# Kernel tuning notes

Hardware: AMD Instinct MI355X
Metric: run time of the kernel (lower is better)

Reference implementation:

```python
import jax, jax.numpy as jnp
import numpy as np
from jax import lax

B, C, P, H = 4, 3, 160, 32          # batch of box patches, channels, patch size, score-net hidden
TEMB = 64                            # time-embedding dim
BETA0, BETA1 = 0.1, 20.0             # subVP SDE beta_min / beta_max
T_EPS = 1e-5                         # integration start time (timesteps=(1e-5, 1))
N_STEPS = 10                         # (1 - eps) / ode_step_size with step_size=0.1


def _conv(x, w, b):
    y = lax.conv_general_dilated(x, w, (1, 1), 'SAME',
                                 dimension_numbers=('NCHW', 'OIHW', 'NCHW'))
    return y + b[None, :, None, None]


def _time_emb(t):
    half = TEMB // 2
    freqs = jnp.exp(-np.log(10000.0) / (half - 1) * jnp.arange(half, dtype=jnp.float32))
    a = t[:, None] * 999.0 * freqs[None, :]   # continuous t scaled as in score_sde
    return jnp.concatenate([jnp.sin(a), jnp.cos(a)], axis=-1)


def _score_net(x, t, params):
    w1, b1, wt, bt, w2, b2, w3, b3 = params
    emb = _time_emb(t) @ wt + bt                       # [B, H]
    h = jax.nn.relu(_conv(x, w1, b1) + emb[:, :, None, None])
    h = jax.nn.relu(_conv(h, w2, b2))
    return _conv(h, w3, b3)


def _drift(x, tvec, params):
    # subVP probability-flow ODE drift: f(x,t) - 0.5 * g(t)^2 * score(x,t)
    bd = BETA1 - BETA0
    beta_t = BETA0 + tvec * bd
    lmc = -0.25 * tvec ** 2 * bd - 0.5 * tvec * BETA0   # log mean coeff
    std = 1.0 - jnp.exp(2.0 * lmc)                      # marginal std
    g2 = beta_t * (1.0 - jnp.exp(4.0 * lmc))            # diffusion^2
    score = _score_net(x, tvec, params) / std[:, None, None, None]
    return -0.5 * beta_t[:, None, None, None] * x - 0.5 * g2[:, None, None, None] * score


def _forward(patches, hs_epsilon, params):
    eps = jnp.broadcast_to(hs_epsilon, patches.shape)   # fixed Rademacher probe
    dt = (1.0 - T_EPS) / N_STEPS

    def rhs(x, t):
        tvec = jnp.ones((x.shape[0],), x.dtype) * t
        # Skilling-Hutchinson divergence: eps^T J eps via one jvp
        drift, jv = jax.jvp(lambda xx: _drift(xx, tvec, params), (x,), (eps,))
        return drift, jnp.sum(jv * eps, axis=(1, 2, 3))

    def step(carry, t0):
        x, lp = carry
        k1x, k1l = rhs(x, t0)
        k2x, k2l = rhs(x + 0.5 * dt * k1x, t0 + 0.5 * dt)
        k3x, k3l = rhs(x + 0.5 * dt * k2x, t0 + 0.5 * dt)
        k4x, k4l = rhs(x + dt * k3x, t0 + dt)
        x = x + (dt / 6.0) * (k1x + 2.0 * k2x + 2.0 * k3x + k4x)
        lp = lp + (dt / 6.0) * (k1l + 2.0 * k2l + 2.0 * k3l + k4l)
        return (x, lp), None

    ts = T_EPS + dt * jnp.arange(N_STEPS, dtype=patches.dtype)
    init = (patches, jnp.zeros((patches.shape[0],), patches.dtype))
    (z, delta_logp), _ = lax.scan(jax.checkpoint(step), init, ts)

    Ndim = float(np.prod(patches.shape[1:]))
    prior_logp = -0.5 * Ndim * np.log(2.0 * np.pi) - 0.5 * jnp.sum(z ** 2, axis=(1, 2, 3))
    bpd = -(prior_logp + delta_logp) / np.log(2.0)
    return bpd / Ndim                                   # per-patch NLL (bits/dim)


def setup_inputs() -> dict:
    key = jax.random.key(0)
    ks = jax.random.split(key, 6)
    s = 0.05
    return {
        'patches': jax.random.normal(ks[0], (B, C, P, P), jnp.float32),
        'hs_epsilon': jnp.sign(jax.random.normal(ks[1], (1, C, P, P), jnp.float32)),
        'w1': jax.random.normal(ks[2], (H, C, 3, 3), jnp.float32) * s,
        'b1': jnp.zeros((H,), jnp.float32),
        'wt': jax.random.normal(ks[3], (TEMB, H), jnp.float32) * s,
        'bt': jnp.zeros((H,), jnp.float32),
        'w2': jax.random.normal(ks[4], (H, H, 3, 3), jnp.float32) * s,
        'b2': jnp.zeros((H,), jnp.float32),
        'w3': jax.random.normal(ks[5], (C, H, 3, 3), jnp.float32) * s,
        'b3': jnp.zeros((C,), jnp.float32),
    }


def reference(patches, hs_epsilon, w1, b1, wt, bt, w2, b2, w3, b3):
    params = (w1, b1, wt, bt, w2, b2, w3, b3)
    return _forward(patches, hs_epsilon, params)
```

## Files before the change

kernel.cpp:

```cpp
#include <hip/hip_runtime.h>
#include <hip/hip_bf16.h>
#include <math.h>

#define PW 160
#define PSQ 25600
#define NB 4
#define NX 307200
#define NDIM 76800

#define TY 10
#define TX 20
#define XH 16
#define XW 26
#define XSZ 416
#define H1H 14
#define H1W 24
#define H1N 336
#define H2H 12
#define H2W 22
#define H2N 264
#define OUTN 200

typedef __attribute__((ext_vector_type(8))) short short8;
typedef __attribute__((ext_vector_type(4))) float float4v;

struct TS40 { float t[40]; };
struct MC40 { float m[40]; float A; };

__device__ __forceinline__ short bf16s(float f) {
    return __builtin_bit_cast(short, __float2bfloat16(f));
}
__device__ __forceinline__ unsigned packbf(float a, float b) {
    return (unsigned)(unsigned short)bf16s(a) | ((unsigned)(unsigned short)bf16s(b) << 16);
}

__global__ void emb_kernel(const float* __restrict__ wt, const float* __restrict__ bt,
                           float* __restrict__ emb, TS40 ts) {
    int r = blockIdx.x, k = threadIdx.x;
    __shared__ float e64[64];
    float t = ts.t[r];
    int j = k & 31;
    float freq = expf(-0.29710775393471556f * (float)j);
    float a = t * 999.0f * freq;
    e64[k] = (k < 32) ? sinf(a) : cosf(a);
    __syncthreads();
    if (k < 32) {
        float acc = bt[k];
        #pragma unroll 8
        for (int q = 0; q < 64; q++) acc += e64[q] * wt[q * 32 + k];
        emb[r * 32 + k] = acc;
    }
}

__global__ void repack_kernel(const float* __restrict__ w1, const float* __restrict__ w2,
                              const float* __restrict__ w3, short* __restrict__ w1p,
                              short* __restrict__ w2p, short* __restrict__ w3p) {
    int tid = blockIdx.x * 256 + threadIdx.x;
    if (tid < 9216) {
        int j = tid & 7, co = (tid >> 3) & 31, q4 = tid >> 8;
        int tap = q4 >> 2, quad = q4 & 3, ci = quad * 8 + j;
        w2p[tid] = bf16s(w2[(co * 32 + ci) * 9 + tap]);
    }
    if (tid < 4608) {
        int j = tid & 7, co = (tid >> 3) & 15, q4 = tid >> 7;
        int tap = q4 >> 2, quad = q4 & 3, ci = quad * 8 + j;
        float v = (co < 3) ? w3[(co * 32 + ci) * 9 + tap] : 0.0f;
        w3p[tid] = bf16s(v);
    }
    if (tid < 1024) {
        int j = tid & 7, co = (tid >> 3) & 31, quad = tid >> 8;
        int k = quad * 8 + j;
        float v = 0.0f;
        if (k < 27) { int tap = (k * 11) >> 5; int ci = k - tap * 3; v = w1[(co * 3 + ci) * 9 + tap]; }
        w1p[tid] = bf16s(v);
    }
}

__global__ __launch_bounds__(256) void teps_conv1(
    const float* __restrict__ xin, const short* __restrict__ w1p,
    short* __restrict__ outH) {
    const int tile = blockIdx.x;
    const int ty0 = (tile / 10) * 16, tx0 = (tile % 10) * 16;
    const int tid = threadIdx.x;
    const int lane = tid & 63, wv = tid >> 6;
    const int n = lane & 15, quad = lane >> 4;
    __shared__ float sX[3 * 324];
    for (int idx = tid; idx < 3 * 324; idx += 256) {
        int ci = idx / 324, p = idx - ci * 324;
        int ly = p / 18, lx = p - ly * 18;
        int gy = ty0 + ly - 1, gx = tx0 + lx - 1;
        float v = 0.0f;
        if (gy >= 0 && gy < PW && gx >= 0 && gx < PW)
            v = xin[(size_t)ci * PSQ + gy * PW + gx];
        sX[idx] = v;
    }
    __syncthreads();
    int offj[8], valj[8];
    #pragma unroll
    for (int j = 0; j < 8; ++j) {
        int k = quad * 8 + j;
        valj[j] = (k < 27);
        int tap = (k * 11) >> 5; if (k >= 27) tap = 0;
        int ci = k - tap * 3;
        int dy = (tap * 11) >> 5, dx = tap - dy * 3;
        offj[j] = valj[j] ? (ci * 324 + dy * 18 + dx + n) : 0;
    }
    short8 a0 = *(const short8*)&w1p[(quad * 32 + n) * 8];
    short8 a1 = *(const short8*)&w1p[(quad * 32 + 16 + n) * 8];
    #pragma unroll
    for (int r = 0; r < 4; ++r) {
        int row = wv * 4 + r;
        short8 bb;
        #pragma unroll
        for (int j = 0; j < 8; ++j) {
            float v = valj[j] ? sX[offj[j] + row * 18] : 0.0f;
            bb[j] = bf16s(v);
        }
        float4v acc0 = {0.f, 0.f, 0.f, 0.f}, acc1 = {0.f, 0.f, 0.f, 0.f};
        acc0 = __builtin_amdgcn_mfma_f32_16x16x32_bf16(a0, bb, acc0, 0, 0, 0);
        acc1 = __builtin_amdgcn_mfma_f32_16x16x32_bf16(a1, bb, acc1, 0, 0, 0);
        int pix = (ty0 + row) * PW + tx0 + n;
        uint2 h0, h1v;
        h0.x = packbf(acc0[0], acc0[1]); h0.y = packbf(acc0[2], acc0[3]);
        h1v.x = packbf(acc1[0], acc1[1]); h1v.y = packbf(acc1[2], acc1[3]);
        *(uint2*)&outH[(size_t)pix * 32 + quad * 4] = h0;
        *(uint2*)&outH[(size_t)pix * 32 + 16 + quad * 4] = h1v;
    }
}

__global__ __launch_bounds__(256, 2) void fused_stage(
    const float* __restrict__ xin, float* __restrict__ x0,
    float* __restrict__ xacc, float* __restrict__ xst,
    const short* __restrict__ w1p, const short* __restrict__ w2p,
    const short* __restrict__ w3p, const float* __restrict__ b1,
    const float* __restrict__ b2, const float* __restrict__ b3,
    const float* __restrict__ embr, const short* __restrict__ tepsb,
    const float* __restrict__ epsin, float* __restrict__ Sacc,
    float c1, float c2, float dt, int mode) {
    const int bid = blockIdx.x;
    const int tile = ((bid & 7) << 4) | (bid >> 3);
    const int b = blockIdx.y;
    const int oy = (tile >> 3) * TY, ox = (tile & 7) * TX;
    const int tid = threadIdx.x;
    const int lane = tid & 63, wv = tid >> 6;
    const int n = lane & 15, quad = lane >> 4;

    __shared__ __align__(16) char smem[77088];
    short* sH1 = (short*)smem;
    short* sD1 = (short*)(smem + 21504);
    short* sH2 = (short*)(smem + 43008);
    short* sD2 = (short*)(smem + 59904);
    short* sX  = (short*)(smem + 43008);
    float* sOut = (float*)smem;
    float* sBE = (float*)(smem + 76800);
    float* sB2 = (float*)(smem + 76928);
    float* sB3 = (float*)(smem + 77056);
    float* wsum = (float*)(smem + 77068);

    if (tid < 32) { sBE[tid] = b1[tid] + embr[tid]; sB2[tid] = b2[tid]; }
    if (tid < 3) sB3[tid] = b3[tid];

    for (int idx = tid; idx < 3 * XSZ; idx += 256) {
        int ci = idx / XSZ, p = idx - ci * XSZ;
        int ly = p / XW, lx = p - ly * XW;
        int gy = oy - 3 + ly, gx = ox - 3 + lx;
        float v = 0.0f;
        if (gy >= 0 && gy < PW && gx >= 0 && gx < PW)
            v = xin[(size_t)(b * 3 + ci) * PSQ + gy * PW + gx];
        sX[idx] = bf16s(v);
    }
    __syncthreads();

    {
        int koff[8], kval[8];
        #pragma unroll
        for (int j = 0; j < 8; ++j) {
            int k = quad * 8 + j;
            kval[j] = (k < 27);
            int tap = (k * 11) >> 5; if (k >= 27) tap = 0;
            int ci = k - tap * 3;
            int dy = (tap * 11) >> 5, dx = tap - dy * 3;
            koff[j] = kval[j] ? (ci * XSZ + dy * XW + dx) : 0;
        }
        short8 a0 = *(const short8*)&w1p[(quad * 32 + n) * 8];
        short8 a1 = *(const short8*)&w1p[(quad * 32 + 16 + n) * 8];
        for (int t = wv; t < 21; t += 4) {
            int p = t * 16 + n;
            int ry = p / H1W, rx = p - ry * H1W;
            int gy = oy - 2 + ry, gx = ox - 2 + rx;
            int inimg = (gy >= 0 && gy < PW && gx >= 0 && gx < PW);
            size_t tbase = inimg ? ((size_t)(gy * PW + gx) * 32) : 0;
            uint2 t20 = *(const uint2*)&tepsb[tbase + quad * 4];
            uint2 t21 = *(const uint2*)&tepsb[tbase + 16 + quad * 4];
            int base = ry * XW + rx;
            short8 bb;
            #pragma unroll
            for (int j = 0; j < 8; ++j)
                bb[j] = kval[j] ? sX[koff[j] + base] : (short)0;
            float4v acc0 = {0.f, 0.f, 0.f, 0.f}, acc1 = {0.f, 0.f, 0.f, 0.f};
            acc0 = __builtin_amdgcn_mfma_f32_16x16x32_bf16(a0, bb, acc0, 0, 0, 0);
            acc1 = __builtin_amdgcn_mfma_f32_16x16x32_bf16(a1, bb, acc1, 0, 0, 0);
            int swz = (p & 7) << 4;
            #pragma unroll
            for (int mt = 0; mt < 2; ++mt) {
                float4v* ac = mt ? &acc1 : &acc0;
                uint2 t2 = mt ? t21 : t20;
                int co0 = mt * 16 + quad * 4;
                unsigned ts4[4] = {t2.x & 0xFFFFu, t2.x >> 16, t2.y & 0xFFFFu, t2.y >> 16};
                unsigned hv[4], dv[4];
                #pragma unroll
                for (int g = 0; g < 4; ++g) {
                    float pre = (*ac)[g] + sBE[co0 + g];
                    hv[g] = inimg ? (unsigned)(unsigned short)bf16s(fmaxf(pre, 0.0f)) : 0u;
                    dv[g] = (inimg && pre > 0.0f) ? ts4[g] : 0u;
                }
                uint2 hw, dw;
                hw.x = hv[0] | (hv[1] << 16); hw.y = hv[2] | (hv[3] << 16);
                dw.x = dv[0] | (dv[1] << 16); dw.y = dv[2] | (dv[3] << 16);
                int byw = ((p << 6) | (co0 << 1)) ^ swz;
                *(uint2*)((char*)sH1 + byw) = hw;
                *(uint2*)((char*)sD1 + byw) = dw;
            }
        }
    }
    __syncthreads();

    {
        short8 a2[9][2];
        #pragma unroll
        for (int tap = 0; tap < 9; ++tap) {
            a2[tap][0] = *(const short8*)&w2p[((tap * 4 + quad) * 32 + n) * 8];
            a2[tap][1] = *(const short8*)&w2p[((tap * 4 + quad) * 32 + 16 + n) * 8];
        }
        for (int t = wv; t < 17; t += 4) {
            int p = t * 16 + n;
            int pc = p < H2N ? p : (H2N - 1);
            int ry = pc / H2W, rx = pc - ry * H2W;
            float4v aP0 = {0.f,0.f,0.f,0.f}, aP1 = {0.f,0.f,0.f,0.f};
            float4v aD0 = {0.f,0.f,0.f,0.f}, aD1 = {0.f,0.f,0.f,0.f};
            #pragma unroll
            for (int tap = 0; tap < 9; ++tap) {
                int dy = (tap * 11) >> 5, dx = tap - dy * 3;
                int q = (ry + dy) * H1W + rx + dx;
                int byr = ((q << 6) | (quad << 4)) ^ ((q & 7) << 4);
                short8 bp = *(const short8*)((const char*)sH1 + byr);
                short8 bd = *(const short8*)((const char*)sD1 + byr);
                aP0 = __builtin_amdgcn_mfma_f32_16x16x32_bf16(a2[tap][0], bp, aP0, 0, 0, 0);
                aP1 = __builtin_amdgcn_mfma_f32_16x16x32_bf16(a2[tap][1], bp, aP1, 0, 0, 0);
                aD0 = __builtin_amdgcn_mfma_f32_16x16x32_bf16(a2[tap][0], bd, aD0, 0, 0, 0);
                aD1 = __builtin_amdgcn_mfma_f32_16x16x32_bf16(a2[tap][1], bd, aD1, 0, 0, 0);
            }
            int gy = oy - 1 + ry, gx = ox - 1 + rx;
            int inimg = (gy >= 0 && gy < PW && gx >= 0 && gx < PW);
            if (p < H2N) {
                int swz = (p & 7) << 4;
                #pragma unroll
                for (int mt = 0; mt < 2; ++mt) {
                    float4v* acP = mt ? &aP1 : &aP0;
                    float4v* acD = mt ? &aD1 : &aD0;
                    int co0 = mt * 16 + quad * 4;
                    unsigned hv[4], dv[4];
                    #pragma unroll
                    for (int g = 0; g < 4; ++g) {
                        float pre = (*acP)[g] + sB2[co0 + g];
                        hv[g] = inimg ? (unsigned)(unsigned short)bf16s(fmaxf(pre, 0.0f)) : 0u;
                        dv[g] = (inimg && pre > 0.0f) ? (unsigned)(unsigned short)bf16s((*acD)[g]) : 0u;
                    }
                    uint2 hw, dw;
                    hw.x = hv[0] | (hv[1] << 16); hw.y = hv[2] | (hv[3] << 16);
                    dw.x = dv[0] | (dv[1] << 16); dw.y = dv[2] | (dv[3] << 16);
                    int byw = ((p << 6) | (co0 << 1)) ^ swz;
                    *(uint2*)((char*)sH2 + byw) = hw;
                    *(uint2*)((char*)sD2 + byw) = dw;
                }
            }
        }
    }
    __syncthreads();

    float pf_x[3], pf_e[3], pf_a[3], pf_x0[3];
    #pragma unroll
    for (int rep = 0; rep < 3; ++rep) {
        int idx = tid + rep * 256;
        int v = (idx < 3 * OUTN);
        int idc = v ? idx : 0;
        int c = idc / OUTN, pp = idc - c * OUTN;
        int ry = pp / TX, rx = pp - ry * TX;
        int pix = (oy + ry) * PW + ox + rx;
        size_t gi = (size_t)(b * 3 + c) * PSQ + pix;
        pf_x[rep] = v ? xin[gi] : 0.0f;
        pf_e[rep] = v ? epsin[c * PSQ + pix] : 0.0f;
        pf_a[rep] = 0.0f; pf_x0[rep] = 0.0f;
        if (mode >= 1) {
            pf_a[rep] = v ? xacc[gi] : 0.0f;
            pf_x0[rep] = v ? x0[gi] : 0.0f;
        }
    }

    {
        short8 a3[9];
        #pragma unroll
        for (int tap = 0; tap < 9; ++tap)
            a3[tap] = *(const short8*)&w3p[((tap * 4 + quad) * 16 + n) * 8];
        for (int t = wv; t < 13; t += 4) {
            int p = t * 16 + n;
            int pc = p < OUTN ? p : (OUTN - 1);
            int ry = pc / TX, rx = pc - ry * TX;
            float4v aP = {0.f,0.f,0.f,0.f}, aD = {0.f,0.f,0.f,0.f};
            #pragma unroll
            for (int tap = 0; tap < 9; ++tap) {
                int dy = (tap * 11) >> 5, dx = tap - dy * 3;
                int q = (ry + dy) * H2W + rx + dx;
                int byr = ((q << 6) | (quad << 4)) ^ ((q & 7) << 4);
                short8 bp = *(const short8*)((const char*)sH2 + byr);
                short8 bd = *(const short8*)((const char*)sD2 + byr);
                aP = __builtin_amdgcn_mfma_f32_16x16x32_bf16(a3[tap], bp, aP, 0, 0, 0);
                aD = __builtin_amdgcn_mfma_f32_16x16x32_bf16(a3[tap], bd, aD, 0, 0, 0);
            }
            if (quad == 0 && p < OUTN) {
                #pragma unroll
                for (int c = 0; c < 3; ++c) {
                    sOut[c * OUTN + p] = aP[c] + sB3[c];
                    sOut[3 * OUTN + c * OUTN + p] = aD[c];
                }
            }
        }
    }
    __syncthreads();

    float s = 0.0f;
    #pragma unroll
    for (int rep = 0; rep < 3; ++rep) {
        int idx = tid + rep * 256;
        if (idx < 3 * OUTN) {
            int c = idx / OUTN, pp = idx - c * OUTN;
            int ry = pp / TX, rx = pp - ry * TX;
            int pix = (oy + ry) * PW + ox + rx;
            size_t gi = (size_t)(b * 3 + c) * PSQ + pix;
            float y = sOut[c * OUTN + pp];
            float d = sOut[3 * OUTN + c * OUTN + pp];
            float xv = pf_x[rep];
            float k = -c1 * xv - c2 * y;
            if (mode == 0) {
                xacc[gi] = k;
                xst[gi] = xv + 0.5f * dt * k;
            } else if (mode == 1) {
                xacc[gi] = pf_a[rep] + 2.0f * k;
                xst[gi] = pf_x0[rep] + 0.5f * dt * k;
            } else if (mode == 2) {
                xacc[gi] = pf_a[rep] + 2.0f * k;
                xst[gi] = pf_x0[rep] + dt * k;
            } else {
                x0[gi] = pf_x0[rep] + (dt / 6.0f) * (pf_a[rep] + k);
            }
            s += d * pf_e[rep];
        }
    }
    #pragma unroll
    for (int off = 32; off > 0; off >>= 1) s += __shfl_down(s, off);
    if (lane == 0) wsum[wv] = s;
    __syncthreads();
    if (tid == 0) atomicAdd(&Sacc[b], wsum[0] + wsum[1] + wsum[2] + wsum[3]);
}

__global__ void sumz2_kernel(const float* __restrict__ x0, float* __restrict__ sumz2) {
    int b = blockIdx.x, seg = blockIdx.y, tid = threadIdx.x;
    const float* p = x0 + (size_t)b * NDIM + seg * 3072;
    float s = 0.0f;
    for (int i = tid; i < 3072; i += 256) { float v = p[i]; s += v * v; }
    #pragma unroll
    for (int off = 32; off > 0; off >>= 1) s += __shfl_down(s, off);
    __shared__ float wsum[4];
    if ((tid & 63) == 0) wsum[tid >> 6] = s;
    __syncthreads();
    if (tid == 0) atomicAdd(&sumz2[b], wsum[0] + wsum[1] + wsum[2] + wsum[3]);
}

__global__ void bpd_kernel(const float* __restrict__ S, const float* __restrict__ sumz2,
                           float* __restrict__ out, MC40 mc) {
    int b = threadIdx.x;
    if (b >= NB) return;
    float lp = mc.A;
    for (int r = 0; r < 40; r++) lp -= mc.m[r] * S[r * 4 + b];
    float prior = -70574.479354f - 0.5f * sumz2[b];
    out[b] = -(prior + lp) * 1.8785164100960743e-5f;
}

extern "C" void kernel_launch(void* const* d_in, const int* in_sizes, int n_in,
                              void* d_out, int out_size, void* d_ws, size_t ws_size,
                              hipStream_t stream) {
    const float* patches = (const float*)d_in[0];
    const float* epsin = (const float*)d_in[1];
    const float* w1 = (const float*)d_in[2];
    const float* b1 = (const float*)d_in[3];
    const float* wt = (const float*)d_in[4];
    const float* bt = (const float*)d_in[5];
    const float* w2 = (const float*)d_in[6];
    const float* b2 = (const float*)d_in[7];
    const float* w3 = (const float*)d_in[8];
    const float* b3 = (const float*)d_in[9];
    float* outp = (float*)d_out;
    char* wsb = (char*)d_ws;

    float* Sbuf  = (float*)(wsb + 0);
    float* sumz2 = (float*)(wsb + 640);
    float* emb   = (float*)(wsb + 1024);
    short* w1p   = (short*)(wsb + 6144);
    short* w2p   = (short*)(wsb + 8192);
    short* w3p   = (short*)(wsb + 26624);
    short* tepsb = (short*)(wsb + 36864);
    float* x0    = (float*)(wsb + 1675264);
    float* xacc  = (float*)(wsb + 2904064);
    float* xst   = (float*)(wsb + 4132864);

    const double dt = (1.0 - 1e-5) / 10.0;
    TS40 ts; MC40 mc;
    float c1a[40], c2a[40];
    double A = 0.0;
    const double wgt[4] = {1.0, 2.0, 2.0, 1.0};
    for (int i = 0; i < 10; i++) {
        double t0 = 1e-5 + dt * i;
        double tr[4] = {t0, t0 + 0.5 * dt, t0 + 0.5 * dt, t0 + dt};
        for (int s = 0; s < 4; s++) {
            int r = i * 4 + s;
            double t = tr[s];
            double beta = 0.1 + 19.9 * t;
            double lmc = -0.25 * t * t * 19.9 - 0.05 * t;
            double stdv = 1.0 - exp(2.0 * lmc);
            double g2 = beta * (1.0 - exp(4.0 * lmc));
            double c2 = 0.5 * g2 / stdv;
            ts.t[r] = (float)t;
            c1a[r] = (float)(0.5 * beta);
            c2a[r] = (float)c2;
            double coef = dt / 6.0 * wgt[s];
            mc.m[r] = (float)(coef * c2);
            A += coef * (-0.5 * beta * (double)NDIM);
        }
    }
    mc.A = (float)A;

    hipMemsetAsync(wsb, 0, 656, stream);
    hipMemcpyAsync(x0, patches, NX * sizeof(float), hipMemcpyDeviceToDevice, stream);

    emb_kernel<<<40, 64, 0, stream>>>(wt, bt, emb, ts);
    repack_kernel<<<36, 256, 0, stream>>>(w1, w2, w3, w1p, w2p, w3p);
    teps_conv1<<<100, 256, 0, stream>>>(epsin, w1p, tepsb);

    for (int i = 0; i < 10; i++) {
        for (int s = 0; s < 4; s++) {
            int r = i * 4 + s;
            const float* xin = (s == 0) ? x0 : xst;
            fused_stage<<<dim3(128, NB), 256, 0, stream>>>(
                xin, x0, xacc, xst, w1p, w2p, w3p, b1, b2, b3,
                emb + r * 32, tepsb, epsin, Sbuf + r * 4,
                c1a[r], c2a[r], (float)dt, s);
        }
    }
    sumz2_kernel<<<dim3(NB, 25), 256, 0, stream>>>(x0, sumz2);
    bpd_kernel<<<1, 64, 0, stream>>>(Sbuf, sumz2, outp, mc);
}
```

Before: 948.3 us.

## Fuse all RK4 stages into one persistent kernel with grid barriers

Replaces the 40 per-stage launches with a single persistent kernel of 512 blocks. Blocks synchronise between stages through an atomic counter barrier in global memory. Weights, the conv1 tangent (eps) result and the eps values are loaded once into registers and reused across all stages, and the separate teps_conv1 kernel is removed. This cuts launch overhead and repeated weight loads, but it relies on all 512 blocks being co-resident and adds spin-wait barrier cost plus register pressure.

Measured after the change: 3.790 ms. 300% more time.

```diff
diff --git a/kernel.cpp b/kernel.cpp
--- a/kernel.cpp
+++ b/kernel.cpp
@@ -7,16 +7,13 @@
 #define NB 4
 #define NX 307200
 #define NDIM 76800
+#define NBLK 512
 
 #define TY 10
 #define TX 20
-#define XH 16
 #define XW 26
 #define XSZ 416
-#define H1H 14
 #define H1W 24
-#define H1N 336
-#define H2H 12
 #define H2W 22
 #define H2N 264
 #define OUTN 200
@@ -26,6 +23,7 @@
 
 struct TS40 { float t[40]; };
 struct MC40 { float m[40]; float A; };
+struct PK { float c1[40]; float c2[40]; };
 
 __device__ __forceinline__ short bf16s(float f) {
     return __builtin_bit_cast(short, __float2bfloat16(f));
@@ -76,67 +74,14 @@
     }
 }
 
-__global__ __launch_bounds__(256) void teps_conv1(
-    const float* __restrict__ xin, const short* __restrict__ w1p,
-    short* __restrict__ outH) {
-    const int tile = blockIdx.x;
-    const int ty0 = (tile / 10) * 16, tx0 = (tile % 10) * 16;
-    const int tid = threadIdx.x;
-    const int lane = tid & 63, wv = tid >> 6;
-    const int n = lane & 15, quad = lane >> 4;
-    __shared__ float sX[3 * 324];
-    for (int idx = tid; idx < 3 * 324; idx += 256) {
-        int ci = idx / 324, p = idx - ci * 324;
-        int ly = p / 18, lx = p - ly * 18;
-        int gy = ty0 + ly - 1, gx = tx0 + lx - 1;
-        float v = 0.0f;
-        if (gy >= 0 && gy < PW && gx >= 0 && gx < PW)
-            v = xin[(size_t)ci * PSQ + gy * PW + gx];
-        sX[idx] = v;
-    }
-    __syncthreads();
-    int offj[8], valj[8];
-    #pragma unroll
-    for (int j = 0; j < 8; ++j) {
-        int k = quad * 8 + j;
-        valj[j] = (k < 27);
-        int tap = (k * 11) >> 5; if (k >= 27) tap = 0;
-        int ci = k - tap * 3;
-        int dy = (tap * 11) >> 5, dx = tap - dy * 3;
-        offj[j] = valj[j] ? (ci * 324 + dy * 18 + dx + n) : 0;
-    }
-    short8 a0 = *(const short8*)&w1p[(quad * 32 + n) * 8];
-    short8 a1 = *(const short8*)&w1p[(quad * 32 + 16 + n) * 8];
-    #pragma unroll
-    for (int r = 0; r < 4; ++r) {
-        int row = wv * 4 + r;
-        short8 bb;
-        #pragma unroll
-        for (int j = 0; j < 8; ++j) {
-            float v = valj[j] ? sX[offj[j] + row * 18] : 0.0f;
-            bb[j] = bf16s(v);
-        }
-        float4v acc0 = {0.f, 0.f, 0.f, 0.f}, acc1 = {0.f, 0.f, 0.f, 0.f};
-        acc0 = __builtin_amdgcn_mfma_f32_16x16x32_bf16(a0, bb, acc0, 0, 0, 0);
-        acc1 = __builtin_amdgcn_mfma_f32_16x16x32_bf16(a1, bb, acc1, 0, 0, 0);
-        int pix = (ty0 + row) * PW + tx0 + n;
-        uint2 h0, h1v;
-        h0.x = packbf(acc0[0], acc0[1]); h0.y = packbf(acc0[2], acc0[3]);
-        h1v.x = packbf(acc1[0], acc1[1]); h1v.y = packbf(acc1[2], acc1[3]);
-        *(uint2*)&outH[(size_t)pix * 32 + quad * 4] = h0;
-        *(uint2*)&outH[(size_t)pix * 32 + 16 + quad * 4] = h1v;
-    }
-}
-
-__global__ __launch_bounds__(256, 2) void fused_stage(
-    const float* __restrict__ xin, float* __restrict__ x0,
-    float* __restrict__ xacc, float* __restrict__ xst,
+__global__ __launch_bounds__(256, 2) void persist_kernel(
+    float* __restrict__ x0, float* __restrict__ xacc, float* __restrict__ xst,
     const short* __restrict__ w1p, const short* __restrict__ w2p,
     const short* __restrict__ w3p, const float* __restrict__ b1,
     const float* __restrict__ b2, const float* __restrict__ b3,
-    const float* __restrict__ embr, const short* __restrict__ tepsb,
-    const float* __restrict__ epsin, float* __restrict__ Sacc,
-    float c1, float c2, float dt, int mode) {
+    const float* __restrict__ emb, const float* __restrict__ epsin,
+    float* __restrict__ Sacc, unsigned* __restrict__ bars,
+    PK pk, float dt) {
     const int bid = blockIdx.x;
     const int tile = ((bid & 7) << 4) | (bid >> 3);
     const int b = blockIdx.y;
@@ -157,8 +102,22 @@
     float* sB3 = (float*)(smem + 77056);
     float* wsum = (float*)(smem + 77068);
 
-    if (tid < 32) { sBE[tid] = b1[tid] + embr[tid]; sB2[tid] = b2[tid]; }
+    float myb1 = (tid < 32) ? b1[tid] : 0.0f;
+    if (tid < 32) sB2[tid] = b2[tid];
     if (tid < 3) sB3[tid] = b3[tid];
+
+    int koff[8], kval[8];
+    #pragma unroll
+    for (int j = 0; j < 8; ++j) {
+        int k = quad * 8 + j;
+        kval[j] = (k < 27);
+        int tap = (k * 11) >> 5; if (k >= 27) tap = 0;
+        int ci = k - tap * 3;
+        int dy = (tap * 11) >> 5, dx = tap - dy * 3;
+        koff[j] = kval[j] ? (ci * XSZ + dy * XW + dx) : 0;
+    }
+    short8 a0 = *(const short8*)&w1p[(quad * 32 + n) * 8];
+    short8 a1w = *(const short8*)&w1p[(quad * 32 + 16 + n) * 8];
 
     for (int idx = tid; idx < 3 * XSZ; idx += 256) {
         int ci = idx / XSZ, p = idx - ci * XSZ;
@@ -166,32 +125,19 @@
         int gy = oy - 3 + ly, gx = ox - 3 + lx;
         float v = 0.0f;
         if (gy >= 0 && gy < PW && gx >= 0 && gx < PW)
-            v = xin[(size_t)(b * 3 + ci) * PSQ + gy * PW + gx];
+            v = epsin[(size_t)ci * PSQ + gy * PW + gx];
         sX[idx] = bf16s(v);
     }
     __syncthreads();
-
-    {
-        int koff[8], kval[8];
-        #pragma unroll
-        for (int j = 0; j < 8; ++j) {
-            int k = quad * 8 + j;
-            kval[j] = (k < 27);
-            int tap = (k * 11) >> 5; if (k >= 27) tap = 0;
-            int ci = k - tap * 3;
-            int dy = (tap * 11) >> 5, dx = tap - dy * 3;
-            koff[j] = kval[j] ? (ci * XSZ + dy * XW + dx) : 0;
-        }
-        short8 a0 = *(const short8*)&w1p[(quad * 32 + n) * 8];
-        short8 a1 = *(const short8*)&w1p[(quad * 32 + 16 + n) * 8];
-        for (int t = wv; t < 21; t += 4) {
+    uint2 pt0[6], pt1[6];
+    #pragma unroll
+    for (int it = 0; it < 6; ++it) { pt0[it].x = pt0[it].y = 0u; pt1[it].x = pt1[it].y = 0u; }
+    #pragma unroll
+    for (int it = 0; it < 6; ++it) {
+        int t = wv + it * 4;
+        if (t < 21) {
             int p = t * 16 + n;
             int ry = p / H1W, rx = p - ry * H1W;
-            int gy = oy - 2 + ry, gx = ox - 2 + rx;
-            int inimg = (gy >= 0 && gy < PW && gx >= 0 && gx < PW);
-            size_t tbase = inimg ? ((size_t)(gy * PW + gx) * 32) : 0;
-            uint2 t20 = *(const uint2*)&tepsb[tbase + quad * 4];
-            uint2 t21 = *(const uint2*)&tepsb[tbase + 16 + quad * 4];
             int base = ry * XW + rx;
             short8 bb;
             #pragma unroll
@@ -199,39 +145,94 @@
                 bb[j] = kval[j] ? sX[koff[j] + base] : (short)0;
             float4v acc0 = {0.f, 0.f, 0.f, 0.f}, acc1 = {0.f, 0.f, 0.f, 0.f};
             acc0 = __builtin_amdgcn_mfma_f32_16x16x32_bf16(a0, bb, acc0, 0, 0, 0);
-            acc1 = __builtin_amdgcn_mfma_f32_16x16x32_bf16(a1, bb, acc1, 0, 0, 0);
-            int swz = (p & 7) << 4;
-            #pragma unroll
-            for (int mt = 0; mt < 2; ++mt) {
-                float4v* ac = mt ? &acc1 : &acc0;
-                uint2 t2 = mt ? t21 : t20;
-                int co0 = mt * 16 + quad * 4;
-                unsigned ts4[4] = {t2.x & 0xFFFFu, t2.x >> 16, t2.y & 0xFFFFu, t2.y >> 16};
-                unsigned hv[4], dv[4];
+            acc1 = __builtin_amdgcn_mfma_f32_16x16x32_bf16(a1w, bb, acc1, 0, 0, 0);
+            pt0[it].x = packbf(acc0[0], acc0[1]); pt0[it].y = packbf(acc0[2], acc0[3]);
+            pt1[it].x = packbf(acc1[0], acc1[1]); pt1[it].y = packbf(acc1[2], acc1[3]);
+        }
+    }
+    __syncthreads();
+
+    float pf_e[3];
+    #pragma unroll
+    for (int rep = 0; rep < 3; ++rep) {
+        int idx = tid + rep * 256;
+        int v = (idx < 3 * OUTN);
+        int idc = v ? idx : 0;
+        int c = idc / OUTN, pp = idc - c * OUTN;
+        int ry = pp / TX, rx = pp - ry * TX;
+        pf_e[rep] = v ? epsin[(size_t)c * PSQ + (oy + ry) * PW + ox + rx] : 0.0f;
+    }
+
+    short8 a2[9][2];
+    #pragma unroll
+    for (int tap = 0; tap < 9; ++tap) {
+        a2[tap][0] = *(const short8*)&w2p[((tap * 4 + quad) * 32 + n) * 8];
+        a2[tap][1] = *(const short8*)&w2p[((tap * 4 + quad) * 32 + 16 + n) * 8];
+    }
+    short8 a3[9];
+    #pragma unroll
+    for (int tap = 0; tap < 9; ++tap)
+        a3[tap] = *(const short8*)&w3p[((tap * 4 + quad) * 16 + n) * 8];
+
+    #pragma unroll 1
+    for (int r = 0; r < 40; ++r) {
+        const int mode = r & 3;
+        const float c1 = pk.c1[r], c2 = pk.c2[r];
+        const float* xin = (mode == 0) ? x0 : xst;
+        if (tid < 32) sBE[tid] = myb1 + emb[r * 32 + tid];
+
+        for (int idx = tid; idx < 3 * XSZ; idx += 256) {
+            int ci = idx / XSZ, p = idx - ci * XSZ;
+            int ly = p / XW, lx = p - ly * XW;
+            int gy = oy - 3 + ly, gx = ox - 3 + lx;
+            float v = 0.0f;
+            if (gy >= 0 && gy < PW && gx >= 0 && gx < PW)
+                v = xin[(size_t)(b * 3 + ci) * PSQ + gy * PW + gx];
+            sX[idx] = bf16s(v);
+        }
+        __syncthreads();
+
+        #pragma unroll
+        for (int it = 0; it < 6; ++it) {
+            int t = wv + it * 4;
+            if (t < 21) {
+                int p = t * 16 + n;
+                int ry = p / H1W, rx = p - ry * H1W;
+                int gy = oy - 2 + ry, gx = ox - 2 + rx;
+                int inimg = (gy >= 0 && gy < PW && gx >= 0 && gx < PW);
+                int base = ry * XW + rx;
+                short8 bb;
                 #pragma unroll
-                for (int g = 0; g < 4; ++g) {
-                    float pre = (*ac)[g] + sBE[co0 + g];
-                    hv[g] = inimg ? (unsigned)(unsigned short)bf16s(fmaxf(pre, 0.0f)) : 0u;
-                    dv[g] = (inimg && pre > 0.0f) ? ts4[g] : 0u;
+                for (int j = 0; j < 8; ++j)
+                    bb[j] = kval[j] ? sX[koff[j] + base] : (short)0;
+                float4v acc0 = {0.f, 0.f, 0.f, 0.f}, acc1 = {0.f, 0.f, 0.f, 0.f};
+                acc0 = __builtin_amdgcn_mfma_f32_16x16x32_bf16(a0, bb, acc0, 0, 0, 0);
+                acc1 = __builtin_amdgcn_mfma_f32_16x16x32_bf16(a1w, bb, acc1, 0, 0, 0);
+                int swz = (p & 7) << 4;
+                #pragma unroll
+                for (int mt = 0; mt < 2; ++mt) {
+                    float4v* ac = mt ? &acc1 : &acc0;
+                    uint2 t2 = mt ? pt1[it] : pt0[it];
+                    int co0 = mt * 16 + quad * 4;
+                    unsigned ts4[4] = {t2.x & 0xFFFFu, t2.x >> 16, t2.y & 0xFFFFu, t2.y >> 16};
+                    unsigned hv[4], dv[4];
+                    #pragma unroll
+                    for (int g = 0; g < 4; ++g) {
+                        float pre = (*ac)[g] + sBE[co0 + g];
+                        hv[g] = inimg ? (unsigned)(unsigned short)bf16s(fmaxf(pre, 0.0f)) : 0u;
+                        dv[g] = (inimg && pre > 0.0f) ? ts4[g] : 0u;
+                    }
+                    uint2 hw, dw;
+                    hw.x = hv[0] | (hv[1] << 16); hw.y = hv[2] | (hv[3] << 16);
+                    dw.x = dv[0] | (dv[1] << 16); dw.y = dv[2] | (dv[3] << 16);
+                    int byw = ((p << 6) | (co0 << 1)) ^ swz;
+                    *(uint2*)((char*)sH1 + byw) = hw;
+                    *(uint2*)((char*)sD1 + byw) = dw;
                 }
-                uint2 hw, dw;
-                hw.x = hv[0] | (hv[1] << 16); hw.y = hv[2] | (hv[3] << 16);
-                dw.x = dv[0] | (dv[1] << 16); dw.y = dv[2] | (dv[3] << 16);
-                int byw = ((p << 6) | (co0 << 1)) ^ swz;
-                *(uint2*)((char*)sH1 + byw) = hw;
-                *(uint2*)((char*)sD1 + byw) = dw;
-            }
-        }
-    }
-    __syncthreads();
-
-    {
-        short8 a2[9][2];
-        #pragma unroll
-        for (int tap = 0; tap < 9; ++tap) {
-            a2[tap][0] = *(const short8*)&w2p[((tap * 4 + quad) * 32 + n) * 8];
-            a2[tap][1] = *(const short8*)&w2p[((tap * 4 + quad) * 32 + 16 + n) * 8];
-        }
+            }
+        }
+        __syncthreads();
+
         for (int t = wv; t < 17; t += 4) {
             int p = t * 16 + n;
             int pc = p < H2N ? p : (H2N - 1);
@@ -275,33 +276,25 @@
                 }
             }
         }
-    }
-    __syncthreads();
-
-    float pf_x[3], pf_e[3], pf_a[3], pf_x0[3];
-    #pragma unroll
-    for (int rep = 0; rep < 3; ++rep) {
-        int idx = tid + rep * 256;
-        int v = (idx < 3 * OUTN);
-        int idc = v ? idx : 0;
-        int c = idc / OUTN, pp = idc - c * OUTN;
-        int ry = pp / TX, rx = pp - ry * TX;
-        int pix = (oy + ry) * PW + ox + rx;
-        size_t gi = (size_t)(b * 3 + c) * PSQ + pix;
-        pf_x[rep] = v ? xin[gi] : 0.0f;
-        pf_e[rep] = v ? epsin[c * PSQ + pix] : 0.0f;
-        pf_a[rep] = 0.0f; pf_x0[rep] = 0.0f;
-        if (mode >= 1) {
-            pf_a[rep] = v ? xacc[gi] : 0.0f;
-            pf_x0[rep] = v ? x0[gi] : 0.0f;
-        }
-    }
-
-    {
-        short8 a3[9];
+        __syncthreads();
+
+        float pf_x[3], pf_a[3], pf_x0[3];
         #pragma unroll
-        for (int tap = 0; tap < 9; ++tap)
-            a3[tap] = *(const short8*)&w3p[((tap * 4 + quad) * 16 + n) * 8];
+        for (int rep = 0; rep < 3; ++rep) {
+            int idx = tid + rep * 256;
+            int v = (idx < 3 * OUTN);
+            int idc = v ? idx : 0;
+            int c = idc / OUTN, pp = idc - c * OUTN;
+            int ry = pp / TX, rx = pp - ry * TX;
+            size_t gi = (size_t)(b * 3 + c) * PSQ + (oy + ry) * PW + ox + rx;
+            pf_x[rep] = v ? xin[gi] : 0.0f;
+            pf_a[rep] = 0.0f; pf_x0[rep] = 0.0f;
+            if (mode >= 1) {
+                pf_a[rep] = v ? xacc[gi] : 0.0f;
+                pf_x0[rep] = v ? x0[gi] : 0.0f;
+            }
+        }
+
         for (int t = wv; t < 13; t += 4) {
             int p = t * 16 + n;
             int pc = p < OUTN ? p : (OUTN - 1);
@@ -325,42 +318,53 @@
                 }
             }
         }
-    }
-    __syncthreads();
-
-    float s = 0.0f;
-    #pragma unroll
-    for (int rep = 0; rep < 3; ++rep) {
-        int idx = tid + rep * 256;
-        if (idx < 3 * OUTN) {
-            int c = idx / OUTN, pp = idx - c * OUTN;
-            int ry = pp / TX, rx = pp - ry * TX;
-            int pix = (oy + ry) * PW + ox + rx;
-            size_t gi = (size_t)(b * 3 + c) * PSQ + pix;
-            float y = sOut[c * OUTN + pp];
-            float d = sOut[3 * OUTN + c * OUTN + pp];
-            float xv = pf_x[rep];
-            float k = -c1 * xv - c2 * y;
-            if (mode == 0) {
-                xacc[gi] = k;
-                xst[gi] = xv + 0.5f * dt * k;
-            } else if (mode == 1) {
-                xacc[gi] = pf_a[rep] + 2.0f * k;
-                xst[gi] = pf_x0[rep] + 0.5f * dt * k;
-            } else if (mode == 2) {
-                xacc[gi] = pf_a[rep] + 2.0f * k;
-                xst[gi] = pf_x0[rep] + dt * k;
-            } else {
-                x0[gi] = pf_x0[rep] + (dt / 6.0f) * (pf_a[rep] + k);
-            }
-            s += d * pf_e[rep];
-        }
-    }
-    #pragma unroll
-    for (int off = 32; off > 0; off >>= 1) s += __shfl_down(s, off);
-    if (lane == 0) wsum[wv] = s;
-    __syncthreads();
-    if (tid == 0) atomicAdd(&Sacc[b], wsum[0] + wsum[1] + wsum[2] + wsum[3]);
+        __syncthreads();
+
+        float s = 0.0f;
+        #pragma unroll
+        for (int rep = 0; rep < 3; ++rep) {
+            int idx = tid + rep * 256;
+            if (idx < 3 * OUTN) {
+                int c = idx / OUTN, pp = idx - c * OUTN;
+                int ry = pp / TX, rx = pp - ry * TX;
+                size_t gi = (size_t)(b * 3 + c) * PSQ + (oy + ry) * PW + ox + rx;
+                float y = sOut[c * OUTN + pp];
+                float d = sOut[3 * OUTN + c * OUTN + pp];
+                float xv = pf_x[rep];
+                float k = -c1 * xv - c2 * y;
+                if (mode == 0) {
+                    xacc[gi] = k;
+                    xst[gi] = xv + 0.5f * dt * k;
+                } else if (mode == 1) {
+                    xacc[gi] = pf_a[rep] + 2.0f * k;
+                    xst[gi] = pf_x0[rep] + 0.5f * dt * k;
+                } else if (mode == 2) {
+                    xacc[gi] = pf_a[rep] + 2.0f * k;
+                    xst[gi] = pf_x0[rep] + dt * k;
+                } else {
+                    x0[gi] = pf_x0[rep] + (dt / 6.0f) * (pf_a[rep] + k);
+                }
+                s += d * pf_e[rep];
+            }
+        }
+        #pragma unroll
+        for (int off = 32; off > 0; off >>= 1) s += __shfl_down(s, off);
+        if (lane == 0) wsum[wv] = s;
+        __syncthreads();
+        if (tid == 0) atomicAdd(&Sacc[r * 4 + b], wsum[0] + wsum[1] + wsum[2] + wsum[3]);
+
+        if (r < 39) {
+            __syncthreads();
+            if (tid == 0) {
+                __threadfence();
+                __hip_atomic_fetch_add(&bars[r], 1u, __ATOMIC_ACQ_REL, __HIP_MEMORY_SCOPE_AGENT);
+                while (__hip_atomic_load(&bars[r], __ATOMIC_ACQUIRE, __HIP_MEMORY_SCOPE_AGENT) < NBLK)
+                    __builtin_amdgcn_s_sleep(8);
+                __threadfence();
+            }
+            __syncthreads();
+        }
+    }
 }
 
 __global__ void sumz2_kernel(const float* __restrict__ x0, float* __restrict__ sumz2) {
@@ -404,18 +408,17 @@
 
     float* Sbuf  = (float*)(wsb + 0);
     float* sumz2 = (float*)(wsb + 640);
+    unsigned* bars = (unsigned*)(wsb + 768);
     float* emb   = (float*)(wsb + 1024);
     short* w1p   = (short*)(wsb + 6144);
     short* w2p   = (short*)(wsb + 8192);
     short* w3p   = (short*)(wsb + 26624);
-    short* tepsb = (short*)(wsb + 36864);
     float* x0    = (float*)(wsb + 1675264);
     float* xacc  = (float*)(wsb + 2904064);
     float* xst   = (float*)(wsb + 4132864);
 
     const double dt = (1.0 - 1e-5) / 10.0;
-    TS40 ts; MC40 mc;
-    float c1a[40], c2a[40];
+    TS40 ts; MC40 mc; PK pk;
     double A = 0.0;
     const double wgt[4] = {1.0, 2.0, 2.0, 1.0};
     for (int i = 0; i < 10; i++) {
@@ -430,8 +433,8 @@
             double g2 = beta * (1.0 - exp(4.0 * lmc));
             double c2 = 0.5 * g2 / stdv;
             ts.t[r] = (float)t;
-            c1a[r] = (float)(0.5 * beta);
-            c2a[r] = (float)c2;
+            pk.c1[r] = (float)(0.5 * beta);
+            pk.c2[r] = (float)c2;
             double coef = dt / 6.0 * wgt[s];
             mc.m[r] = (float)(coef * c2);
             A += coef * (-0.5 * beta * (double)NDIM);
@@ -439,23 +442,16 @@
     }
     mc.A = (float)A;
 
-    hipMemsetAsync(wsb, 0, 656, stream);
+    hipMemsetAsync(wsb, 0, 928, stream);
     hipMemcpyAsync(x0, patches, NX * sizeof(float), hipMemcpyDeviceToDevice, stream);
 
     emb_kernel<<<40, 64, 0, stream>>>(wt, bt, emb, ts);
     repack_kernel<<<36, 256, 0, stream>>>(w1, w2, w3, w1p, w2p, w3p);
-    teps_conv1<<<100, 256, 0, stream>>>(epsin, w1p, tepsb);
-
-    for (int i = 0; i < 10; i++) {
-        for (int s = 0; s < 4; s++) {
-            int r = i * 4 + s;
-            const float* xin = (s == 0) ? x0 : xst;
-            fused_stage<<<dim3(128, NB), 256, 0, stream>>>(
-                xin, x0, xacc, xst, w1p, w2p, w3p, b1, b2, b3,
-                emb + r * 32, tepsb, epsin, Sbuf + r * 4,
-                c1a[r], c2a[r], (float)dt, s);
-        }
-    }
+
+    persist_kernel<<<dim3(128, NB), 256, 0, stream>>>(
+        x0, xacc, xst, w1p, w2p, w3p, b1, b2, b3,
+        emb, epsin, Sbuf, bars, pk, (float)dt);
+
     sumz2_kernel<<<dim3(NB, 25), 256, 0, stream>>>(x0, sumz2);
     bpd_kernel<<<1, 64, 0, stream>>>(Sbuf, sumz2, outp, mc);
 }
```

## Double fused stage block to 512 threads and prefetch conv1 tangent loads

Applied to the files above, without the earlier changes.

Raises the fused RK stage kernel from 4 to 8 waves per block and redistributes the conv1/conv2/conv3 tile loops and epilogue across them. The tangent-conv1 global loads are hoisted to the kernel start so they overlap the input staging into shared memory. The aim is more latency hiding inside each block. The launch bound now asks for 4 blocks of 512 threads, which tightens register budgets and may force spills, and the ~77KB of shared memory per block still limits how many blocks fit per CU.

Result: faster. 858.9 us (-9.4%).

```diff
diff --git a/kernel.cpp b/kernel.cpp
--- a/kernel.cpp
+++ b/kernel.cpp
@@ -10,13 +10,9 @@
 
 #define TY 10
 #define TX 20
-#define XH 16
 #define XW 26
 #define XSZ 416
-#define H1H 14
 #define H1W 24
-#define H1N 336
-#define H2H 12
 #define H2W 22
 #define H2N 264
 #define OUTN 200
@@ -128,7 +124,7 @@
     }
 }
 
-__global__ __launch_bounds__(256, 2) void fused_stage(
+__global__ __launch_bounds__(512, 4) void fused_stage(
     const float* __restrict__ xin, float* __restrict__ x0,
     float* __restrict__ xacc, float* __restrict__ xst,
     const short* __restrict__ w1p, const short* __restrict__ w2p,
@@ -145,7 +141,7 @@
     const int lane = tid & 63, wv = tid >> 6;
     const int n = lane & 15, quad = lane >> 4;
 
-    __shared__ __align__(16) char smem[77088];
+    __shared__ __align__(16) char smem[77104];
     short* sH1 = (short*)smem;
     short* sD1 = (short*)(smem + 21504);
     short* sH2 = (short*)(smem + 43008);
@@ -155,12 +151,26 @@
     float* sBE = (float*)(smem + 76800);
     float* sB2 = (float*)(smem + 76928);
     float* sB3 = (float*)(smem + 77056);
-    float* wsum = (float*)(smem + 77068);
+    float* wsum = (float*)(smem + 77072);
+
+    uint2 pt0[3], pt1[3];
+    #pragma unroll
+    for (int it = 0; it < 3; ++it) {
+        int t = wv + it * 8;
+        int tt = (t < 21) ? t : 0;
+        int p = tt * 16 + n;
+        int ry = p / H1W, rx = p - ry * H1W;
+        int gy = oy - 2 + ry, gx = ox - 2 + rx;
+        int ok = (t < 21) && gy >= 0 && gy < PW && gx >= 0 && gx < PW;
+        size_t tbase = ok ? ((size_t)(gy * PW + gx) * 32) : 0;
+        pt0[it] = *(const uint2*)&tepsb[tbase + quad * 4];
+        pt1[it] = *(const uint2*)&tepsb[tbase + 16 + quad * 4];
+    }
 
     if (tid < 32) { sBE[tid] = b1[tid] + embr[tid]; sB2[tid] = b2[tid]; }
     if (tid < 3) sB3[tid] = b3[tid];
 
-    for (int idx = tid; idx < 3 * XSZ; idx += 256) {
+    for (int idx = tid; idx < 3 * XSZ; idx += 512) {
         int ci = idx / XSZ, p = idx - ci * XSZ;
         int ly = p / XW, lx = p - ly * XW;
         int gy = oy - 3 + ly, gx = ox - 3 + lx;
@@ -184,42 +194,43 @@
         }
         short8 a0 = *(const short8*)&w1p[(quad * 32 + n) * 8];
         short8 a1 = *(const short8*)&w1p[(quad * 32 + 16 + n) * 8];
-        for (int t = wv; t < 21; t += 4) {
-            int p = t * 16 + n;
-            int ry = p / H1W, rx = p - ry * H1W;
-            int gy = oy - 2 + ry, gx = ox - 2 + rx;
-            int inimg = (gy >= 0 && gy < PW && gx >= 0 && gx < PW);
-            size_t tbase = inimg ? ((size_t)(gy * PW + gx) * 32) : 0;
-            uint2 t20 = *(const uint2*)&tepsb[tbase + quad * 4];
-            uint2 t21 = *(const uint2*)&tepsb[tbase + 16 + quad * 4];
-            int base = ry * XW + rx;
-            short8 bb;
-            #pragma unroll
-            for (int j = 0; j < 8; ++j)
-                bb[j] = kval[j] ? sX[koff[j] + base] : (short)0;
-            float4v acc0 = {0.f, 0.f, 0.f, 0.f}, acc1 = {0.f, 0.f, 0.f, 0.f};
-            acc0 = __builtin_amdgcn_mfma_f32_16x16x32_bf16(a0, bb, acc0, 0, 0, 0);
-            acc1 = __builtin_amdgcn_mfma_f32_16x16x32_bf16(a1, bb, acc1, 0, 0, 0);
-            int swz = (p & 7) << 4;
-            #pragma unroll
-            for (int mt = 0; mt < 2; ++mt) {
-                float4v* ac = mt ? &acc1 : &acc0;
-                uint2 t2 = mt ? t21 : t20;
-                int co0 = mt * 16 + quad * 4;
-                unsigned ts4[4] = {t2.x & 0xFFFFu, t2.x >> 16, t2.y & 0xFFFFu, t2.y >> 16};
-                unsigned hv[4], dv[4];
+        #pragma unroll
+        for (int it = 0; it < 3; ++it) {
+            int t = wv + it * 8;
+            if (t < 21) {
+                int p = t * 16 + n;
+                int ry = p / H1W, rx = p - ry * H1W;
+                int gy = oy - 2 + ry, gx = ox - 2 + rx;
+                int inimg = (gy >= 0 && gy < PW && gx >= 0 && gx < PW);
+                int base = ry * XW + rx;
+                short8 bb;
                 #pragma unroll
-                for (int g = 0; g < 4; ++g) {
-                    float pre = (*ac)[g] + sBE[co0 + g];
-                    hv[g] = inimg ? (unsigned)(unsigned short)bf16s(fmaxf(pre, 0.0f)) : 0u;
-                    dv[g] = (inimg && pre > 0.0f) ? ts4[g] : 0u;
+                for (int j = 0; j < 8; ++j)
+                    bb[j] = kval[j] ? sX[koff[j] + base] : (short)0;
+                float4v acc0 = {0.f, 0.f, 0.f, 0.f}, acc1 = {0.f, 0.f, 0.f, 0.f};
+                acc0 = __builtin_amdgcn_mfma_f32_16x16x32_bf16(a0, bb, acc0, 0, 0, 0);
+                acc1 = __builtin_amdgcn_mfma_f32_16x16x32_bf16(a1, bb, acc1, 0, 0, 0);
+                int swz = (p & 7) << 4;
+                #pragma unroll
+                for (int mt = 0; mt < 2; ++mt) {
+                    float4v* ac = mt ? &acc1 : &acc0;
+                    uint2 t2 = mt ? pt1[it] : pt0[it];
+                    int co0 = mt * 16 + quad * 4;
+                    unsigned ts4[4] = {t2.x & 0xFFFFu, t2.x >> 16, t2.y & 0xFFFFu, t2.y >> 16};
+                    unsigned hv[4], dv[4];
+                    #pragma unroll
+                    for (int g = 0; g < 4; ++g) {
+                        float pre = (*ac)[g] + sBE[co0 + g];
+                        hv[g] = inimg ? (unsigned)(unsigned short)bf16s(fmaxf(pre, 0.0f)) : 0u;
+                        dv[g] = (inimg && pre > 0.0f) ? ts4[g] : 0u;
+                    }
+                    uint2 hw, dw;
+                    hw.x = hv[0] | (hv[1] << 16); hw.y = hv[2] | (hv[3] << 16);
+                    dw.x = dv[0] | (dv[1] << 16); dw.y = dv[2] | (dv[3] << 16);
+                    int byw = ((p << 6) | (co0 << 1)) ^ swz;
+                    *(uint2*)((char*)sH1 + byw) = hw;
+                    *(uint2*)((char*)sD1 + byw) = dw;
                 }
-                uint2 hw, dw;
-                hw.x = hv[0] | (hv[1] << 16); hw.y = hv[2] | (hv[3] << 16);
-                dw.x = dv[0] | (dv[1] << 16); dw.y = dv[2] | (dv[3] << 16);
-                int byw = ((p << 6) | (co0 << 1)) ^ swz;
-                *(uint2*)((char*)sH1 + byw) = hw;
-                *(uint2*)((char*)sD1 + byw) = dw;
             }
         }
     }
@@ -232,7 +243,7 @@
             a2[tap][0] = *(const short8*)&w2p[((tap * 4 + quad) * 32 + n) * 8];
             a2[tap][1] = *(const short8*)&w2p[((tap * 4 + quad) * 32 + 16 + n) * 8];
         }
-        for (int t = wv; t < 17; t += 4) {
+        for (int t = wv; t < 17; t += 8) {
             int p = t * 16 + n;
             int pc = p < H2N ? p : (H2N - 1);
             int ry = pc / H2W, rx = pc - ry * H2W;
@@ -278,10 +289,10 @@
     }
     __syncthreads();
 
-    float pf_x[3], pf_e[3], pf_a[3], pf_x0[3];
-    #pragma unroll
-    for (int rep = 0; rep < 3; ++rep) {
-        int idx = tid + rep * 256;
+    float pf_x[2], pf_e[2], pf_a[2], pf_x0[2];
+    #pragma unroll
+    for (int rep = 0; rep < 2; ++rep) {
+        int idx = tid + rep * 512;
         int v = (idx < 3 * OUTN);
         int idc = v ? idx : 0;
         int c = idc / OUTN, pp = idc - c * OUTN;
@@ -302,7 +313,7 @@
         #pragma unroll
         for (int tap = 0; tap < 9; ++tap)
             a3[tap] = *(const short8*)&w3p[((tap * 4 + quad) * 16 + n) * 8];
-        for (int t = wv; t < 13; t += 4) {
+        for (int t = wv; t < 13; t += 8) {
             int p = t * 16 + n;
             int pc = p < OUTN ? p : (OUTN - 1);
             int ry = pc / TX, rx = pc - ry * TX;
@@ -330,8 +341,8 @@
 
     float s = 0.0f;
     #pragma unroll
-    for (int rep = 0; rep < 3; ++rep) {
-        int idx = tid + rep * 256;
+    for (int rep = 0; rep < 2; ++rep) {
+        int idx = tid + rep * 512;
         if (idx < 3 * OUTN) {
             int c = idx / OUTN, pp = idx - c * OUTN;
             int ry = pp / TX, rx = pp - ry * TX;
@@ -360,7 +371,12 @@
     for (int off = 32; off > 0; off >>= 1) s += __shfl_down(s, off);
     if (lane == 0) wsum[wv] = s;
     __syncthreads();
-    if (tid == 0) atomicAdd(&Sacc[b], wsum[0] + wsum[1] + wsum[2] + wsum[3]);
+    if (tid == 0) {
+        float tot = 0.0f;
+        #pragma unroll
+        for (int w = 0; w < 8; ++w) tot += wsum[w];
+        atomicAdd(&Sacc[b], tot);
+    }
 }
 
 __global__ void sumz2_kernel(const float* __restrict__ x0, float* __restrict__ sumz2) {
@@ -450,7 +466,7 @@
         for (int s = 0; s < 4; s++) {
             int r = i * 4 + s;
             const float* xin = (s == 0) ? x0 : xst;
-            fused_stage<<<dim3(128, NB), 256, 0, stream>>>(
+            fused_stage<<<dim3(128, NB), 512, 0, stream>>>(
                 xin, x0, xacc, xst, w1p, w2p, w3p, b1, b2, b3,
                 emb + r * 32, tepsb, epsin, Sbuf + r * 4,
                 c1a[r], c2a[r], (float)dt, s);
```
